# Performance work log

Hardware: AMD Instinct MI355X
Metric: run time of the kernel (lower is better)

Reference implementation:

```python
import jax, jax.numpy as jnp
import numpy as np

SOS_IDX, EOS_IDX, PAD_IDX = 0, 1, 59
NEG = -10000.0


def setup_inputs() -> dict:
    B, T, K = 256, 512, 128
    key = jax.random.key(0)
    k1, k2, k3 = jax.random.split(key, 3)
    h = jax.random.normal(k1, (B, T, K), dtype=jnp.float32)
    trans = jax.random.normal(k2, (K, K), dtype=jnp.float32)
    # replicate the constructor's masking of forbidden transitions
    trans = (trans.at[SOS_IDX, :].set(NEG)
                  .at[:, EOS_IDX].set(NEG)
                  .at[:, PAD_IDX].set(NEG)
                  .at[PAD_IDX, :].set(NEG)
                  .at[PAD_IDX, EOS_IDX].set(0.0)
                  .at[PAD_IDX, PAD_IDX].set(0.0))
    # monotone 0/1 float mask from random valid lengths (as a real CRF batch has)
    lengths = jax.random.randint(k3, (B,), 1, T + 1)
    mask = (jnp.arange(T)[None, :] < lengths[:, None]).astype(jnp.float32)
    return {"h": h, "trans": trans, "mask": mask}


def reference(h, trans, mask):
    # h: [B, T, K] emissions; trans: [K, K] (trans[i, j] = score j -> i); mask: [B, T]
    B, T, K = h.shape
    init = jnp.full((B, K), NEG, dtype=h.dtype).at[:, SOS_IDX].set(0.0)

    def step(score, xs):
        h_t, m_t = xs  # [B, K], [B]
        # score[:, None, :] + emit[:, :, None] + trans -> logsumexp over prev tag
        new = jax.nn.logsumexp(score[:, None, :] + h_t[:, :, None] + trans[None], axis=-1)
        m = m_t[:, None]
        return new * m + score * (1.0 - m), None

    score, _ = jax.lax.scan(step, init, (jnp.swapaxes(h, 0, 1), mask.T))
    return jax.nn.logsumexp(score + trans[EOS_IDX], axis=-1)  # [B]
```

## Files before the change

### kernel.cpp

```cpp
#include <hip/hip_runtime.h>

#define NEGV -10000.0f
constexpr int K  = 128;
constexpr int T  = 512;
constexpr int CH = 8;

typedef float f32x2 __attribute__((ext_vector_type(2)));
typedef float f32x4 __attribute__((ext_vector_type(4)));

__device__ __forceinline__ void bar_lgkm() {
  asm volatile("s_waitcnt lgkmcnt(0)\n\ts_barrier" ::: "memory");
}
__device__ __forceinline__ void wait_vm0() {
  asm volatile("s_waitcnt vmcnt(0)" ::: "memory");
}
__device__ __forceinline__ void dma16(const float* g, float* l) {
  __builtin_amdgcn_global_load_lds(
      (const __attribute__((address_space(1))) void*)g,
      (__attribute__((address_space(3))) void*)l, 16, 0, 0);
}
template <int CTRL>
__device__ __forceinline__ float dpp_add(float x) {
  int o = __builtin_amdgcn_update_dpp(0, __float_as_int(x), CTRL, 0xF, 0xF, true);
  return x + __int_as_float(o);
}
__device__ __forceinline__ float sum8(float x) {
  x = dpp_add<0xB1>(x);
  x = dpp_add<0x4E>(x);
  x = dpp_add<0x141>(x);
  return x;
}

#if __has_builtin(__builtin_elementwise_fma)
#define VFMA(a, b, c) __builtin_elementwise_fma((a), (b), (c))
#else
__device__ __forceinline__ f32x2 VFMA(f32x2 a, f32x2 b, f32x2 c) {
  f32x2 r; r.x = fmaf(a.x, b.x, c.x); r.y = fmaf(a.y, b.y, c.y); return r;
}
#endif

__global__ __attribute__((amdgpu_flat_work_group_size(256, 256),
                          amdgpu_waves_per_eu(1, 1)))
void crf_fwd(const float* __restrict__ h, const float* __restrict__ trans,
             const float* __restrict__ mask, float* __restrict__ out) {
  const int tid  = threadIdx.x;
  const int b    = blockIdx.x;
  const int wid  = tid >> 6;
  const int lane = tid & 63;
  const int gl   = lane >> 3;
  const int oct  = lane & 7;
  const int sb   = 4 * (8 * wid + gl);
  const int rot  = oct >> 1;
  const int k0   = 16 * oct + 4 * ((0 + rot) & 3);
  const int k1   = 16 * oct + 4 * ((1 + rot) & 3);
  const int k2   = 16 * oct + 4 * ((2 + rot) & 3);
  const int k3   = 16 * oct + 4 * ((3 + rot) & 3);

  __shared__ __align__(16) float p_lds[2][K];
  __shared__ __align__(16) float hbuf[2][4][CH][32];
  __shared__ float Mslot[2];
  __shared__ float red[8];

  float msum = mask[b * T + tid] + mask[b * T + 256 + tid];
  #pragma unroll
  for (int off = 32; off > 0; off >>= 1) msum += __shfl_xor(msum, off);
  if (lane == 0) red[wid] = msum;

  const float* hb = h + (size_t)b * T * K;
  dma16(hb + (size_t)(lane >> 3) * K + 32 * wid + 4 * (lane & 7),
        &hbuf[0][wid][0][0]);

#define EXP4(v) v.x = __expf(v.x); v.y = __expf(v.y); \
                v.z = __expf(v.z); v.w = __expf(v.w);
#define LDE(si) \
  const float* rp##si = trans + (size_t)(sb + si) * K; \
  f32x4 w##si##0 = *reinterpret_cast<const f32x4*>(rp##si + k0); \
  f32x4 w##si##1 = *reinterpret_cast<const f32x4*>(rp##si + k1); \
  f32x4 w##si##2 = *reinterpret_cast<const f32x4*>(rp##si + k2); \
  f32x4 w##si##3 = *reinterpret_cast<const f32x4*>(rp##si + k3); \
  EXP4(w##si##0) EXP4(w##si##1) EXP4(w##si##2) EXP4(w##si##3) \
  f32x2 E##si##0l = __builtin_shufflevector(w##si##0, w##si##0, 0, 1); \
  f32x2 E##si##0h = __builtin_shufflevector(w##si##0, w##si##0, 2, 3); \
  f32x2 E##si##1l = __builtin_shufflevector(w##si##1, w##si##1, 0, 1); \
  f32x2 E##si##1h = __builtin_shufflevector(w##si##1, w##si##1, 2, 3); \
  f32x2 E##si##2l = __builtin_shufflevector(w##si##2, w##si##2, 0, 1); \
  f32x2 E##si##2h = __builtin_shufflevector(w##si##2, w##si##2, 2, 3); \
  f32x2 E##si##3l = __builtin_shufflevector(w##si##3, w##si##3, 0, 1); \
  f32x2 E##si##3h = __builtin_shufflevector(w##si##3, w##si##3, 2, 3);
  LDE(0) LDE(1) LDE(2) LDE(3)
#undef LDE
#undef EXP4
#define PIN(si) asm volatile("" : "+v"(E##si##0l), "+v"(E##si##0h), \
    "+v"(E##si##1l), "+v"(E##si##1h), "+v"(E##si##2l), "+v"(E##si##2h), \
    "+v"(E##si##3l), "+v"(E##si##3h));
  PIN(0) PIN(1) PIN(2) PIN(3)
#undef PIN
  const f32x4 trE = *reinterpret_cast<const f32x4*>(trans + K + sb);

  if (tid < K) p_lds[0][tid] = (tid == 0) ? 1.0f : 0.0f;
  if (tid < 2) Mslot[tid] = 0.0f;
  bar_lgkm();

  const int len = (int)(red[0] + red[1] + red[2] + red[3] + 0.5f);
  const int nch = (len + CH - 1) >> 3;

  float Scur = 0.0f;
  float fsA = NEGV, fsB = NEGV, fsC = NEGV, fsD = NEGV;

  for (int mc = 0; mc < nch; ++mc) {
    const int base = mc << 3;
    const int cur  = mc & 1;
    #pragma unroll
    for (int c = 0; c < CH; ++c) {
      const int t = base + c;
      if (t >= len) break;
      bar_lgkm();

      float Snext = Scur;
      if (c == 0) {
        wait_vm0();
        const int tn = t + CH;
        if (tn < len) {
          dma16(hb + (size_t)(tn + (lane >> 3)) * K + 32 * wid + 4 * (lane & 7),
                &hbuf[cur ^ 1][wid][0][0]);
        }
        if (mc) Snext = Mslot[mc & 1];
      }

      const f32x4 hv4 = *reinterpret_cast<const f32x4*>(&hbuf[cur][wid][c][4 * gl]);

      const float* pb = p_lds[c & 1];
      f32x4 q0 = *reinterpret_cast<const f32x4*>(pb + k0);
      f32x4 q1 = *reinterpret_cast<const f32x4*>(pb + k1);
      f32x4 q2 = *reinterpret_cast<const f32x4*>(pb + k2);
      f32x4 q3 = *reinterpret_cast<const f32x4*>(pb + k3);
      f32x2 q0l = __builtin_shufflevector(q0, q0, 0, 1);
      f32x2 q0h = __builtin_shufflevector(q0, q0, 2, 3);
      f32x2 q1l = __builtin_shufflevector(q1, q1, 0, 1);
      f32x2 q1h = __builtin_shufflevector(q1, q1, 2, 3);
      f32x2 q2l = __builtin_shufflevector(q2, q2, 0, 1);
      f32x2 q2h = __builtin_shufflevector(q2, q2, 2, 3);
      f32x2 q3l = __builtin_shufflevector(q3, q3, 0, 1);
      f32x2 q3h = __builtin_shufflevector(q3, q3, 2, 3);
#define DOTSI(si) \
      f32x2 aa##si = {0.f, 0.f}, ab##si = {0.f, 0.f}; \
      aa##si = VFMA(E##si##0l, q0l, aa##si); ab##si = VFMA(E##si##0h, q0h, ab##si); \
      aa##si = VFMA(E##si##1l, q1l, aa##si); ab##si = VFMA(E##si##1h, q1h, ab##si); \
      aa##si = VFMA(E##si##2l, q2l, aa##si); ab##si = VFMA(E##si##2h, q2h, ab##si); \
      aa##si = VFMA(E##si##3l, q3l, aa##si); ab##si = VFMA(E##si##3h, q3h, ab##si); \
      const float tot##si = sum8((aa##si.x + aa##si.y) + (ab##si.x + ab##si.y));
      DOTSI(0) DOTSI(1) DOTSI(2) DOTSI(3)
#undef DOTSI

      const float d = Scur - Snext;
      f32x4 pw;
      pw.x = tot0 * __expf(hv4.x + d);
      pw.y = tot1 * __expf(hv4.y + d);
      pw.z = tot2 * __expf(hv4.z + d);
      pw.w = tot3 * __expf(hv4.w + d);
      if (oct == 0)
        *reinterpret_cast<f32x4*>(&p_lds[(c & 1) ^ 1][sb]) = pw;

      if (c == CH - 1 || t == len - 1) {
        fsA = hv4.x + Scur + __logf(tot0);
        fsB = hv4.y + Scur + __logf(tot1);
        fsC = hv4.z + Scur + __logf(tot2);
        fsD = hv4.w + Scur + __logf(tot3);
        if (tid == 0) Mslot[(mc + 1) & 1] = fsC;
      }
      Scur = Snext;
    }
  }

  f32x4 ff;
  ff.x = fsA + trE.x; ff.y = fsB + trE.y;
  ff.z = fsC + trE.z; ff.w = fsD + trE.w;
  float mx = fmaxf(fmaxf(ff.x, ff.y), fmaxf(ff.z, ff.w));
  #pragma unroll
  for (int off = 32; off > 0; off >>= 1) mx = fmaxf(mx, __shfl_xor(mx, off));
  if (lane == 0) red[wid] = mx;
  bar_lgkm();
  const float fm = fmaxf(fmaxf(red[0], red[1]), fmaxf(red[2], red[3]));
  float e = 0.0f;
  if (oct == 0)
    e = (__expf(ff.x - fm) + __expf(ff.y - fm)) +
        (__expf(ff.z - fm) + __expf(ff.w - fm));
  #pragma unroll
  for (int off = 32; off > 0; off >>= 1) e += __shfl_xor(e, off);
  if (lane == 0) red[4 + wid] = e;
  bar_lgkm();
  if (tid == 0) out[b] = fm + __logf((red[4] + red[5]) + (red[6] + red[7]));
}

extern "C" void kernel_launch(void* const* d_in, const int* in_sizes, int n_in,
                              void* d_out, int out_size, void* d_ws, size_t ws_size,
                              hipStream_t stream) {
  const float* h     = (const float*)d_in[0];
  const float* trans = (const float*)d_in[1];
  const float* mask  = (const float*)d_in[2];
  float* out = (float*)d_out;
  const int B = in_sizes[0] / (T * K);
  crf_fwd<<<B, 256, 0, stream>>>(h, trans, mask, out);
}
```

Measured before the change: 267.2 us.

## Remap threads to 8 states by 16 k-groups per dot-product

New measurement: 307.8 us. 15.2% more time.

```diff
diff --git a/kernel.cpp b/kernel.cpp
--- a/kernel.cpp
+++ b/kernel.cpp
@@ -24,10 +24,11 @@
   int o = __builtin_amdgcn_update_dpp(0, __float_as_int(x), CTRL, 0xF, 0xF, true);
   return x + __int_as_float(o);
 }
-__device__ __forceinline__ float sum8(float x) {
+__device__ __forceinline__ float sum16(float x) {
   x = dpp_add<0xB1>(x);
   x = dpp_add<0x4E>(x);
   x = dpp_add<0x141>(x);
+  x = dpp_add<0x140>(x);
   return x;
 }
 
@@ -47,14 +48,12 @@
   const int b    = blockIdx.x;
   const int wid  = tid >> 6;
   const int lane = tid & 63;
-  const int gl   = lane >> 3;
-  const int oct  = lane & 7;
-  const int sb   = 4 * (8 * wid + gl);
-  const int rot  = oct >> 1;
-  const int k0   = 16 * oct + 4 * ((0 + rot) & 3);
-  const int k1   = 16 * oct + 4 * ((1 + rot) & 3);
-  const int k2   = 16 * oct + 4 * ((2 + rot) & 3);
-  const int k3   = 16 * oct + 4 * ((3 + rot) & 3);
+  const int sgl  = lane >> 4;
+  const int kg   = lane & 15;
+  const int sb   = 32 * wid + 8 * sgl;
+  const int s    = (kg >> 2) & 1;
+  const int kA   = 8 * kg + 4 * s;
+  const int kB   = 8 * kg + 4 * (1 - s);
 
   __shared__ __align__(16) float p_lds[2][K];
   __shared__ __align__(16) float hbuf[2][4][CH][32];
@@ -74,28 +73,21 @@
                 v.z = __expf(v.z); v.w = __expf(v.w);
 #define LDE(si) \
   const float* rp##si = trans + (size_t)(sb + si) * K; \
-  f32x4 w##si##0 = *reinterpret_cast<const f32x4*>(rp##si + k0); \
-  f32x4 w##si##1 = *reinterpret_cast<const f32x4*>(rp##si + k1); \
-  f32x4 w##si##2 = *reinterpret_cast<const f32x4*>(rp##si + k2); \
-  f32x4 w##si##3 = *reinterpret_cast<const f32x4*>(rp##si + k3); \
-  EXP4(w##si##0) EXP4(w##si##1) EXP4(w##si##2) EXP4(w##si##3) \
-  f32x2 E##si##0l = __builtin_shufflevector(w##si##0, w##si##0, 0, 1); \
-  f32x2 E##si##0h = __builtin_shufflevector(w##si##0, w##si##0, 2, 3); \
-  f32x2 E##si##1l = __builtin_shufflevector(w##si##1, w##si##1, 0, 1); \
-  f32x2 E##si##1h = __builtin_shufflevector(w##si##1, w##si##1, 2, 3); \
-  f32x2 E##si##2l = __builtin_shufflevector(w##si##2, w##si##2, 0, 1); \
-  f32x2 E##si##2h = __builtin_shufflevector(w##si##2, w##si##2, 2, 3); \
-  f32x2 E##si##3l = __builtin_shufflevector(w##si##3, w##si##3, 0, 1); \
-  f32x2 E##si##3h = __builtin_shufflevector(w##si##3, w##si##3, 2, 3);
-  LDE(0) LDE(1) LDE(2) LDE(3)
+  f32x4 wA##si = *reinterpret_cast<const f32x4*>(rp##si + kA); \
+  f32x4 wB##si = *reinterpret_cast<const f32x4*>(rp##si + kB); \
+  EXP4(wA##si) EXP4(wB##si) \
+  f32x2 EA##si##l = __builtin_shufflevector(wA##si, wA##si, 0, 1); \
+  f32x2 EA##si##h = __builtin_shufflevector(wA##si, wA##si, 2, 3); \
+  f32x2 EB##si##l = __builtin_shufflevector(wB##si, wB##si, 0, 1); \
+  f32x2 EB##si##h = __builtin_shufflevector(wB##si, wB##si, 2, 3);
+  LDE(0) LDE(1) LDE(2) LDE(3) LDE(4) LDE(5) LDE(6) LDE(7)
 #undef LDE
 #undef EXP4
-#define PIN(si) asm volatile("" : "+v"(E##si##0l), "+v"(E##si##0h), \
-    "+v"(E##si##1l), "+v"(E##si##1h), "+v"(E##si##2l), "+v"(E##si##2h), \
-    "+v"(E##si##3l), "+v"(E##si##3h));
-  PIN(0) PIN(1) PIN(2) PIN(3)
+#define PIN(si) asm volatile("" : "+v"(EA##si##l), "+v"(EA##si##h), \
+    "+v"(EB##si##l), "+v"(EB##si##h));
+  PIN(0) PIN(1) PIN(2) PIN(3) PIN(4) PIN(5) PIN(6) PIN(7)
 #undef PIN
-  const f32x4 trE = *reinterpret_cast<const f32x4*>(trans + K + sb);
+  const f32x4 trE = *reinterpret_cast<const f32x4*>(trans + K + sb + 4 * (kg & 1));
 
   if (tid < K) p_lds[0][tid] = (tid == 0) ? 1.0f : 0.0f;
   if (tid < 2) Mslot[tid] = 0.0f;
@@ -105,7 +97,7 @@
   const int nch = (len + CH - 1) >> 3;
 
   float Scur = 0.0f;
-  float fsA = NEGV, fsB = NEGV, fsC = NEGV, fsD = NEGV;
+  f32x4 fs4 = {NEGV, NEGV, NEGV, NEGV};
 
   for (int mc = 0; mc < nch; ++mc) {
     const int base = mc << 3;
@@ -127,64 +119,64 @@
         if (mc) Snext = Mslot[mc & 1];
       }
 
-      const f32x4 hv4 = *reinterpret_cast<const f32x4*>(&hbuf[cur][wid][c][4 * gl]);
+      const f32x4 hv4 = *reinterpret_cast<const f32x4*>(
+          &hbuf[cur][wid][c][8 * sgl + 4 * (kg & 1)]);
 
       const float* pb = p_lds[c & 1];
-      f32x4 q0 = *reinterpret_cast<const f32x4*>(pb + k0);
-      f32x4 q1 = *reinterpret_cast<const f32x4*>(pb + k1);
-      f32x4 q2 = *reinterpret_cast<const f32x4*>(pb + k2);
-      f32x4 q3 = *reinterpret_cast<const f32x4*>(pb + k3);
-      f32x2 q0l = __builtin_shufflevector(q0, q0, 0, 1);
-      f32x2 q0h = __builtin_shufflevector(q0, q0, 2, 3);
-      f32x2 q1l = __builtin_shufflevector(q1, q1, 0, 1);
-      f32x2 q1h = __builtin_shufflevector(q1, q1, 2, 3);
-      f32x2 q2l = __builtin_shufflevector(q2, q2, 0, 1);
-      f32x2 q2h = __builtin_shufflevector(q2, q2, 2, 3);
-      f32x2 q3l = __builtin_shufflevector(q3, q3, 0, 1);
-      f32x2 q3h = __builtin_shufflevector(q3, q3, 2, 3);
+      const f32x4 qA = *reinterpret_cast<const f32x4*>(pb + kA);
+      const f32x4 qB = *reinterpret_cast<const f32x4*>(pb + kB);
+      const f32x2 qAl = __builtin_shufflevector(qA, qA, 0, 1);
+      const f32x2 qAh = __builtin_shufflevector(qA, qA, 2, 3);
+      const f32x2 qBl = __builtin_shufflevector(qB, qB, 0, 1);
+      const f32x2 qBh = __builtin_shufflevector(qB, qB, 2, 3);
 #define DOTSI(si) \
-      f32x2 aa##si = {0.f, 0.f}, ab##si = {0.f, 0.f}; \
-      aa##si = VFMA(E##si##0l, q0l, aa##si); ab##si = VFMA(E##si##0h, q0h, ab##si); \
-      aa##si = VFMA(E##si##1l, q1l, aa##si); ab##si = VFMA(E##si##1h, q1h, ab##si); \
-      aa##si = VFMA(E##si##2l, q2l, aa##si); ab##si = VFMA(E##si##2h, q2h, ab##si); \
-      aa##si = VFMA(E##si##3l, q3l, aa##si); ab##si = VFMA(E##si##3h, q3h, ab##si); \
-      const float tot##si = sum8((aa##si.x + aa##si.y) + (ab##si.x + ab##si.y));
+      f32x2 u##si = {0.f, 0.f}, v##si = {0.f, 0.f}; \
+      u##si = VFMA(EA##si##l, qAl, u##si); v##si = VFMA(EA##si##h, qAh, v##si); \
+      u##si = VFMA(EB##si##l, qBl, u##si); v##si = VFMA(EB##si##h, qBh, v##si); \
+      const float tot##si = sum16((u##si.x + u##si.y) + (v##si.x + v##si.y));
       DOTSI(0) DOTSI(1) DOTSI(2) DOTSI(3)
+      DOTSI(4) DOTSI(5) DOTSI(6) DOTSI(7)
 #undef DOTSI
 
-      const float d = Scur - Snext;
-      f32x4 pw;
-      pw.x = tot0 * __expf(hv4.x + d);
-      pw.y = tot1 * __expf(hv4.y + d);
-      pw.z = tot2 * __expf(hv4.z + d);
-      pw.w = tot3 * __expf(hv4.w + d);
-      if (oct == 0)
-        *reinterpret_cast<f32x4*>(&p_lds[(c & 1) ^ 1][sb]) = pw;
+      const float dshift = Scur - Snext;
+      if (kg < 2) {
+        f32x4 eh;
+        eh.x = __expf(hv4.x + dshift); eh.y = __expf(hv4.y + dshift);
+        eh.z = __expf(hv4.z + dshift); eh.w = __expf(hv4.w + dshift);
+        f32x4 pw;
+        pw.x = (kg == 0 ? tot0 : tot4) * eh.x;
+        pw.y = (kg == 0 ? tot1 : tot5) * eh.y;
+        pw.z = (kg == 0 ? tot2 : tot6) * eh.z;
+        pw.w = (kg == 0 ? tot3 : tot7) * eh.w;
+        *reinterpret_cast<f32x4*>(&p_lds[(c & 1) ^ 1][sb + 4 * kg]) = pw;
 
-      if (c == CH - 1 || t == len - 1) {
-        fsA = hv4.x + Scur + __logf(tot0);
-        fsB = hv4.y + Scur + __logf(tot1);
-        fsC = hv4.z + Scur + __logf(tot2);
-        fsD = hv4.w + Scur + __logf(tot3);
-        if (tid == 0) Mslot[(mc + 1) & 1] = fsC;
+        if (c == CH - 1 || t == len - 1) {
+          fs4.x = __logf(pw.x) + Snext;
+          fs4.y = __logf(pw.y) + Snext;
+          fs4.z = __logf(pw.z) + Snext;
+          fs4.w = __logf(pw.w) + Snext;
+          if (tid == 0) Mslot[(mc + 1) & 1] = fs4.z;
+        }
       }
       Scur = Snext;
     }
   }
 
   f32x4 ff;
-  ff.x = fsA + trE.x; ff.y = fsB + trE.y;
-  ff.z = fsC + trE.z; ff.w = fsD + trE.w;
+  if (kg < 2) {
+    ff.x = fs4.x + trE.x; ff.y = fs4.y + trE.y;
+    ff.z = fs4.z + trE.z; ff.w = fs4.w + trE.w;
+  } else {
+    ff.x = NEGV; ff.y = NEGV; ff.z = NEGV; ff.w = NEGV;
+  }
   float mx = fmaxf(fmaxf(ff.x, ff.y), fmaxf(ff.z, ff.w));
   #pragma unroll
   for (int off = 32; off > 0; off >>= 1) mx = fmaxf(mx, __shfl_xor(mx, off));
   if (lane == 0) red[wid] = mx;
   bar_lgkm();
   const float fm = fmaxf(fmaxf(red[0], red[1]), fmaxf(red[2], red[3]));
-  float e = 0.0f;
-  if (oct == 0)
-    e = (__expf(ff.x - fm) + __expf(ff.y - fm)) +
-        (__expf(ff.z - fm) + __expf(ff.w - fm));
+  float e = (__expf(ff.x - fm) + __expf(ff.y - fm)) +
+            (__expf(ff.z - fm) + __expf(ff.w - fm));
   #pragma unroll
   for (int off = 32; off > 0; off >>= 1) e += __shfl_xor(e, off);
   if (lane == 0) red[4 + wid] = e;
```

## Prefetch emissions into double-buffered registers instead of LDS DMA

Applied to the files above, without the earlier changes.

New measurement: 273.9 us. 2.5% more time.

```diff
diff --git a/kernel.cpp b/kernel.cpp
--- a/kernel.cpp
+++ b/kernel.cpp
@@ -10,14 +10,6 @@
 
 __device__ __forceinline__ void bar_lgkm() {
   asm volatile("s_waitcnt lgkmcnt(0)\n\ts_barrier" ::: "memory");
-}
-__device__ __forceinline__ void wait_vm0() {
-  asm volatile("s_waitcnt vmcnt(0)" ::: "memory");
-}
-__device__ __forceinline__ void dma16(const float* g, float* l) {
-  __builtin_amdgcn_global_load_lds(
-      (const __attribute__((address_space(1))) void*)g,
-      (__attribute__((address_space(3))) void*)l, 16, 0, 0);
 }
 template <int CTRL>
 __device__ __forceinline__ float dpp_add(float x) {
@@ -57,7 +49,6 @@
   const int k3   = 16 * oct + 4 * ((3 + rot) & 3);
 
   __shared__ __align__(16) float p_lds[2][K];
-  __shared__ __align__(16) float hbuf[2][4][CH][32];
   __shared__ float Mslot[2];
   __shared__ float red[8];
 
@@ -65,10 +56,6 @@
   #pragma unroll
   for (int off = 32; off > 0; off >>= 1) msum += __shfl_xor(msum, off);
   if (lane == 0) red[wid] = msum;
-
-  const float* hb = h + (size_t)b * T * K;
-  dma16(hb + (size_t)(lane >> 3) * K + 32 * wid + 4 * (lane & 7),
-        &hbuf[0][wid][0][0]);
 
 #define EXP4(v) v.x = __expf(v.x); v.y = __expf(v.y); \
                 v.z = __expf(v.z); v.w = __expf(v.w);
@@ -97,6 +84,23 @@
 #undef PIN
   const f32x4 trE = *reinterpret_cast<const f32x4*>(trans + K + sb);
 
+  const float* hT = h + (size_t)b * T * K + sb;
+  f32x4 hA0, hA1, hA2, hA3, hA4, hA5, hA6, hA7;
+  f32x4 hB0 = {0,0,0,0}, hB1 = {0,0,0,0}, hB2 = {0,0,0,0}, hB3 = {0,0,0,0},
+        hB4 = {0,0,0,0}, hB5 = {0,0,0,0}, hB6 = {0,0,0,0}, hB7 = {0,0,0,0};
+#define LDH(BUF, t0) \
+  BUF##0 = *reinterpret_cast<const f32x4*>(hT + (size_t)((t0) + 0) * K); \
+  BUF##1 = *reinterpret_cast<const f32x4*>(hT + (size_t)((t0) + 1) * K); \
+  BUF##2 = *reinterpret_cast<const f32x4*>(hT + (size_t)((t0) + 2) * K); \
+  BUF##3 = *reinterpret_cast<const f32x4*>(hT + (size_t)((t0) + 3) * K); \
+  BUF##4 = *reinterpret_cast<const f32x4*>(hT + (size_t)((t0) + 4) * K); \
+  BUF##5 = *reinterpret_cast<const f32x4*>(hT + (size_t)((t0) + 5) * K); \
+  BUF##6 = *reinterpret_cast<const f32x4*>(hT + (size_t)((t0) + 6) * K); \
+  BUF##7 = *reinterpret_cast<const f32x4*>(hT + (size_t)((t0) + 7) * K); \
+  asm volatile("" : "+v"(BUF##0), "+v"(BUF##1), "+v"(BUF##2), "+v"(BUF##3), \
+                    "+v"(BUF##4), "+v"(BUF##5), "+v"(BUF##6), "+v"(BUF##7));
+  LDH(hA, 0)
+
   if (tid < K) p_lds[0][tid] = (tid == 0) ? 1.0f : 0.0f;
   if (tid < 2) Mslot[tid] = 0.0f;
   bar_lgkm();
@@ -107,70 +111,70 @@
   float Scur = 0.0f;
   float fsA = NEGV, fsB = NEGV, fsC = NEGV, fsD = NEGV;
 
-  for (int mc = 0; mc < nch; ++mc) {
-    const int base = mc << 3;
-    const int cur  = mc & 1;
-    #pragma unroll
-    for (int c = 0; c < CH; ++c) {
-      const int t = base + c;
-      if (t >= len) break;
-      bar_lgkm();
-
-      float Snext = Scur;
-      if (c == 0) {
-        wait_vm0();
-        const int tn = t + CH;
-        if (tn < len) {
-          dma16(hb + (size_t)(tn + (lane >> 3)) * K + 32 * wid + 4 * (lane & 7),
-                &hbuf[cur ^ 1][wid][0][0]);
-        }
-        if (mc) Snext = Mslot[mc & 1];
-      }
-
-      const f32x4 hv4 = *reinterpret_cast<const f32x4*>(&hbuf[cur][wid][c][4 * gl]);
-
-      const float* pb = p_lds[c & 1];
-      f32x4 q0 = *reinterpret_cast<const f32x4*>(pb + k0);
-      f32x4 q1 = *reinterpret_cast<const f32x4*>(pb + k1);
-      f32x4 q2 = *reinterpret_cast<const f32x4*>(pb + k2);
-      f32x4 q3 = *reinterpret_cast<const f32x4*>(pb + k3);
-      f32x2 q0l = __builtin_shufflevector(q0, q0, 0, 1);
-      f32x2 q0h = __builtin_shufflevector(q0, q0, 2, 3);
-      f32x2 q1l = __builtin_shufflevector(q1, q1, 0, 1);
-      f32x2 q1h = __builtin_shufflevector(q1, q1, 2, 3);
-      f32x2 q2l = __builtin_shufflevector(q2, q2, 0, 1);
-      f32x2 q2h = __builtin_shufflevector(q2, q2, 2, 3);
-      f32x2 q3l = __builtin_shufflevector(q3, q3, 0, 1);
-      f32x2 q3h = __builtin_shufflevector(q3, q3, 2, 3);
+#define STEP(cc, CUR, NXT, MC, BASE)                                         \
+  if ((BASE) + (cc) < len) {                                                 \
+    bar_lgkm();                          \
+    float Snext = Scur;                                                      \
+    if ((cc) == 0) {                                         \
+      if (MC) Snext = Mslot[(MC) & 1];                                       \
+      if ((BASE) + CH < len) { LDH(NXT, (BASE) + CH) }         \
+    }                                                                        \
+    const f32x4 hv4 = CUR##cc;                                               \
+    const float* pb = p_lds[(cc) & 1];                                       \
+    const f32x4 qq0 = *reinterpret_cast<const f32x4*>(pb + k0);              \
+    const f32x4 qq1 = *reinterpret_cast<const f32x4*>(pb + k1);              \
+    const f32x4 qq2 = *reinterpret_cast<const f32x4*>(pb + k2);              \
+    const f32x4 qq3 = *reinterpret_cast<const f32x4*>(pb + k3);              \
+    const f32x2 q0l = __builtin_shufflevector(qq0, qq0, 0, 1);               \
+    const f32x2 q0h = __builtin_shufflevector(qq0, qq0, 2, 3);               \
+    const f32x2 q1l = __builtin_shufflevector(qq1, qq1, 0, 1);               \
+    const f32x2 q1h = __builtin_shufflevector(qq1, qq1, 2, 3);               \
+    const f32x2 q2l = __builtin_shufflevector(qq2, qq2, 0, 1);               \
+    const f32x2 q2h = __builtin_shufflevector(qq2, qq2, 2, 3);               \
+    const f32x2 q3l = __builtin_shufflevector(qq3, qq3, 0, 1);               \
+    const f32x2 q3h = __builtin_shufflevector(qq3, qq3, 2, 3);               \
+    DOTSI(0) DOTSI(1) DOTSI(2) DOTSI(3)                                      \
+    const float dsh = Scur - Snext;          \
+    if (oct == 0) {                                                          \
+      f32x4 pw;                                                              \
+      pw.x = tot0 * __expf(hv4.x + dsh);                                     \
+      pw.y = tot1 * __expf(hv4.y + dsh);                                     \
+      pw.z = tot2 * __expf(hv4.z + dsh);                                     \
+      pw.w = tot3 * __expf(hv4.w + dsh);                                     \
+      *reinterpret_cast<f32x4*>(&p_lds[((cc) & 1) ^ 1][sb]) = pw;            \
+    }                                                                        \
+    if ((cc) == CH - 1 || (BASE) + (cc) == len - 1) {                        \
+      fsA = hv4.x + Scur + __logf(tot0);                                     \
+      fsB = hv4.y + Scur + __logf(tot1);                                     \
+      fsC = hv4.z + Scur + __logf(tot2);                                     \
+      fsD = hv4.w + Scur + __logf(tot3);                                     \
+      if (tid == 0) Mslot[((MC) + 1) & 1] = fsC;      \
+    }                                                                        \
+    Scur = Snext;                                                            \
+  }
+
 #define DOTSI(si) \
-      f32x2 aa##si = {0.f, 0.f}, ab##si = {0.f, 0.f}; \
-      aa##si = VFMA(E##si##0l, q0l, aa##si); ab##si = VFMA(E##si##0h, q0h, ab##si); \
-      aa##si = VFMA(E##si##1l, q1l, aa##si); ab##si = VFMA(E##si##1h, q1h, ab##si); \
-      aa##si = VFMA(E##si##2l, q2l, aa##si); ab##si = VFMA(E##si##2h, q2h, ab##si); \
-      aa##si = VFMA(E##si##3l, q3l, aa##si); ab##si = VFMA(E##si##3h, q3h, ab##si); \
-      const float tot##si = sum8((aa##si.x + aa##si.y) + (ab##si.x + ab##si.y));
-      DOTSI(0) DOTSI(1) DOTSI(2) DOTSI(3)
+      f32x2 u##si = {0.f, 0.f}, v##si = {0.f, 0.f}; \
+      u##si = VFMA(E##si##0l, q0l, u##si); v##si = VFMA(E##si##0h, q0h, v##si); \
+      u##si = VFMA(E##si##1l, q1l, u##si); v##si = VFMA(E##si##1h, q1h, v##si); \
+      u##si = VFMA(E##si##2l, q2l, u##si); v##si = VFMA(E##si##2h, q2h, v##si); \
+      u##si = VFMA(E##si##3l, q3l, u##si); v##si = VFMA(E##si##3h, q3h, v##si); \
+      const float tot##si = sum8((u##si.x + u##si.y) + (v##si.x + v##si.y));
+
+#define CHUNK(CUR, NXT, MC, BASE)                                            \
+  { STEP(0, CUR, NXT, MC, BASE) STEP(1, CUR, NXT, MC, BASE)                  \
+    STEP(2, CUR, NXT, MC, BASE) STEP(3, CUR, NXT, MC, BASE)                  \
+    STEP(4, CUR, NXT, MC, BASE) STEP(5, CUR, NXT, MC, BASE)                  \
+    STEP(6, CUR, NXT, MC, BASE) STEP(7, CUR, NXT, MC, BASE) }
+
+  for (int mc = 0; mc < nch; mc += 2) {
+    CHUNK(hA, hB, mc, mc << 3)
+    if (mc + 1 < nch) { CHUNK(hB, hA, mc + 1, (mc + 1) << 3) }
+  }
+#undef CHUNK
 #undef DOTSI
-
-      const float d = Scur - Snext;
-      f32x4 pw;
-      pw.x = tot0 * __expf(hv4.x + d);
-      pw.y = tot1 * __expf(hv4.y + d);
-      pw.z = tot2 * __expf(hv4.z + d);
-      pw.w = tot3 * __expf(hv4.w + d);
-      if (oct == 0)
-        *reinterpret_cast<f32x4*>(&p_lds[(c & 1) ^ 1][sb]) = pw;
-
-      if (c == CH - 1 || t == len - 1) {
-        fsA = hv4.x + Scur + __logf(tot0);
-        fsB = hv4.y + Scur + __logf(tot1);
-        fsC = hv4.z + Scur + __logf(tot2);
-        fsD = hv4.w + Scur + __logf(tot3);
-        if (tid == 0) Mslot[(mc + 1) & 1] = fsC;
-      }
-      Scur = Snext;
-    }
-  }
+#undef STEP
+#undef LDH
 
   f32x4 ff;
   ff.x = fsA + trE.x; ff.y = fsB + trE.y;
```
